# Kernel optimization log

Measured on AMD Instinct MI355X. Metric: run time of the kernel, lower is better.

The kernel has to match this reference:

```python
import jax, jax.numpy as jnp
import numpy as np

H = 512      # hidden_size
NH = 8       # num_heads
DH = H // NH # head_dim = 64
NL = 2       # num_layers
R = 64       # number of AST relation types
PAD = 0      # padding relation index
FF = 4 * H   # FFN inner dim
B, T, S = 4, 512, 512
NEG = -1e10
EPS = 1e-5


def layer_norm(x, g, b):
    m = jnp.mean(x, axis=-1, keepdims=True)
    v = jnp.mean((x - m) ** 2, axis=-1, keepdims=True)
    return (x - m) * jax.lax.rsqrt(v + EPS) * g + b


def setup_inputs() -> dict:
    key = jax.random.key(0)
    ks = iter(jax.random.split(key, 40))

    def n(shape, scale=0.02):
        return jax.random.normal(next(ks), shape, dtype=jnp.float32) * scale

    inp = {
        'q': jax.random.normal(next(ks), (B, T, H), dtype=jnp.float32),
        'kv': jax.random.normal(next(ks), (B, S, H), dtype=jnp.float32),
        'rel_emb_k': n((R, DH)).at[PAD].set(0.0),
        'rel_emb_v': n((R, DH)).at[PAD].set(0.0),
        'Wq_s': n((NL, H, H)), 'bq_s': jnp.zeros((NL, H)),
        'Wk_s': n((NL, H, H)), 'Wv_s': n((NL, H, H)),
        'Wo_s': n((NL, H, H)), 'bo_s': jnp.zeros((NL, H)),
        'ln1_g': jnp.ones((NL, H)), 'ln1_b': jnp.zeros((NL, H)),
        'Wq_c': n((NL, H, H)), 'bq_c': jnp.zeros((NL, H)),
        'Wk_c': n((NL, H, H)), 'Wv_c': n((NL, H, H)),
        'Wo_c': n((NL, H, H)), 'bo_c': jnp.zeros((NL, H)),
        'ln2_g': jnp.ones((NL, H)), 'ln2_b': jnp.zeros((NL, H)),
        'W1': n((NL, H, FF)), 'b1': jnp.zeros((NL, FF)),
        'W2': n((NL, FF, H)), 'b2': jnp.zeros((NL, H)),
        'ln3_g': jnp.ones((NL, H)), 'ln3_b': jnp.zeros((NL, H)),
        'rel_ids': jax.random.randint(next(ks), (B, T, T), 0, R),
        'enc_mask': jnp.ones((B, S), dtype=bool),
    }
    return inp


def reference(q, kv, rel_emb_k, rel_emb_v,
              Wq_s, bq_s, Wk_s, Wv_s, Wo_s, bo_s, ln1_g, ln1_b,
              Wq_c, bq_c, Wk_c, Wv_c, Wo_c, bo_c, ln2_g, ln2_b,
              W1, b1, W2, b2, ln3_g, ln3_b,
              rel_ids, enc_mask):
    scale = np.sqrt(DH).astype(np.float32)
    # relation embeddings shared across layers/heads: [B,T,T,DH]
    rel_k = rel_emb_k[rel_ids]
    rel_v = rel_emb_v[rel_ids]
    tril = jnp.tril(jnp.ones((T, T), dtype=bool))
    rel_mask = (rel_ids != PAD) & tril[None]

    o = q
    for i in range(NL):
        # --- relation-aware masked self-attention ---
        Q = (o @ Wq_s[i] + bq_s[i]).reshape(B, T, NH, DH)
        K = (o @ Wk_s[i]).reshape(B, T, NH, DH)
        V = (o @ Wv_s[i]).reshape(B, T, NH, DH)
        # Q . (K + rel_k)^T decomposed to avoid materializing [B,NH,T,T,DH]
        e = (jnp.einsum('blhd,bmhd->bhlm', Q, K)
             + jnp.einsum('blhd,blmd->bhlm', Q, rel_k)) / scale
        e = jnp.where(rel_mask[:, None], e, NEG)
        a = jax.nn.softmax(e, axis=-1)
        att = (jnp.einsum('bhlm,bmhd->blhd', a, V)
               + jnp.einsum('bhlm,blmd->blhd', a, rel_v)).reshape(B, T, H)
        o = layer_norm(o + att @ Wo_s[i] + bo_s[i], ln1_g[i], ln1_b[i])

        # --- cross-attention ---
        Qc = (o @ Wq_c[i] + bq_c[i]).reshape(B, T, NH, DH)
        Kc = (kv @ Wk_c[i]).reshape(B, S, NH, DH)
        Vc = (kv @ Wv_c[i]).reshape(B, S, NH, DH)
        ec = jnp.einsum('bthd,bshd->bhts', Qc, Kc) / scale
        ec = jnp.where(enc_mask[:, None, None, :], ec, NEG)
        ac = jax.nn.softmax(ec, axis=-1)
        oc = jnp.einsum('bhts,bshd->bthd', ac, Vc).reshape(B, T, H)
        o = layer_norm(o + oc @ Wo_c[i] + bo_c[i], ln2_g[i], ln2_b[i])

        # --- feedforward ---
        h = jax.nn.relu(o @ W1[i] + b1[i])
        o = layer_norm(o + h @ W2[i] + b2[i], ln3_g[i], ln3_b[i])
    return o
```

## Files before the change

kernel.cpp:

```cpp
#include <hip/hip_runtime.h>

static constexpr int Hc  = 512;
static constexpr int NHc = 8;
static constexpr int DHc = 64;
static constexpr int NLc = 2;
static constexpr int Rc  = 64;
static constexpr int FFc = 2048;
static constexpr int Bc  = 4;
static constexpr int Tc  = 512;
#define NEGV (-1e10f)
#define EPSV 1e-5f
#define THRV 6.0f

typedef unsigned short u16;
typedef __attribute__((ext_vector_type(8))) short s16x8;
typedef __attribute__((ext_vector_type(4))) float f32x4;

__device__ __forceinline__ f32x4 mfma_bf16(s16x8 a, s16x8 b, f32x4 c) {
  return __builtin_amdgcn_mfma_f32_16x16x32_bf16(a, b, c, 0, 0, 0);
}
__device__ __forceinline__ u16 f2bf(float f) {
  union { float f; unsigned u; } x; x.f = f;
  unsigned r = (x.u + 0x7FFFu + ((x.u >> 16) & 1u)) >> 16;
  return (u16)r;
}
__device__ __forceinline__ float bf2f(u16 h) {
  union { unsigned u; float f; } x; x.u = ((unsigned)h) << 16;
  return x.f;
}
__device__ __forceinline__ unsigned cvtpk(float a, float b) {
  unsigned r;
  asm("v_cvt_pk_bf16_f32 %0, %1, %2" : "=v"(r) : "v"(a), "v"(b));
  return r;
}

template <int BM, int BN, bool RELU, int OUT>
__global__ __launch_bounds__(256) void gemm_mfma(
    const u16* __restrict__ A, const u16* __restrict__ Wt,
    const float* __restrict__ bias, int biasN,
    void* __restrict__ Cout, int N, int K) {
  __shared__ u16 As[BM * 32];
  __shared__ u16 Bs[BN * 32];
  const int tid = threadIdx.x;
  const int w = tid >> 6, lane = tid & 63, g = lane >> 4, li = lane & 15;
  const int bn = blockIdx.x * BN, bm = blockIdx.y * BM;
  const int r0 = (w & 1) * (BM / 2), c0 = (w >> 1) * (BN / 2);
  constexpr int MR = BM / 32, NR = BN / 32;
  f32x4 acc[MR][NR];
#pragma unroll
  for (int i = 0; i < MR; ++i)
#pragma unroll
    for (int j = 0; j < NR; ++j) acc[i][j] = (f32x4){0.f, 0.f, 0.f, 0.f};

  for (int k0 = 0; k0 < K; k0 += 32) {
    __syncthreads();
#pragma unroll
    for (int it = 0; it < BM / 64; ++it) {
      int s = it * 256 + tid;
      int row = s >> 2, ch = s & 3;
      s16x8 v = *(const s16x8*)(A + (size_t)(bm + row) * K + k0 + ch * 8);
      *(s16x8*)&As[row * 32 + ((ch ^ (row & 3)) * 8)] = v;
    }
#pragma unroll
    for (int it = 0; it < BN / 64; ++it) {
      int s = it * 256 + tid;
      int row = s >> 2, ch = s & 3;
      s16x8 v = *(const s16x8*)(Wt + (size_t)(bn + row) * K + k0 + ch * 8);
      *(s16x8*)&Bs[row * 32 + ((ch ^ (row & 3)) * 8)] = v;
    }
    __syncthreads();
    s16x8 ar[MR], br[NR];
#pragma unroll
    for (int i = 0; i < MR; ++i) {
      int row = r0 + i * 16 + li;
      ar[i] = *(const s16x8*)&As[row * 32 + ((g ^ (row & 3)) * 8)];
    }
#pragma unroll
    for (int j = 0; j < NR; ++j) {
      int row = c0 + j * 16 + li;
      br[j] = *(const s16x8*)&Bs[row * 32 + ((g ^ (row & 3)) * 8)];
    }
#pragma unroll
    for (int i = 0; i < MR; ++i)
#pragma unroll
      for (int j = 0; j < NR; ++j) acc[i][j] = mfma_bf16(ar[i], br[j], acc[i][j]);
  }

#pragma unroll
  for (int j = 0; j < NR; ++j) {
    int col = bn + c0 + j * 16 + li;
    float bv = (bias && col < biasN) ? bias[col] : 0.f;
#pragma unroll
    for (int i = 0; i < MR; ++i) {
#pragma unroll
      for (int r = 0; r < 4; ++r) {
        int rowg = bm + r0 + i * 16 + 4 * g + r;
        float v = acc[i][j][r] + bv;
        if (RELU) v = fmaxf(v, 0.f);
        if (OUT == 0) ((float*)Cout)[(size_t)rowg * N + col] = v;
        else          ((u16*)Cout)[(size_t)rowg * N + col] = f2bf(v);
      }
    }
  }
}

struct WPtrs { const float* p[10]; };

__global__ __launch_bounds__(256) void wcvt(WPtrs wp, u16* __restrict__ dst) {
  constexpr int NE = 20;
  constexpr int srcIdx[NE] = {0,1,0,1,3,3,4,4,5,5,6,6,7,7,2,2,8,8,9,9};
  constexpr int srcOff[NE] = {0,0,262144,262144,0,262144,0,262144,0,262144,
                              0,262144,0,262144,0,262144,0,1048576,0,1048576};
  constexpr int dstOff[NE] = {0,262144,524288,786432,1048576,1310720,
                              1572864,1835008,2097152,2359296,2621440,2883584,
                              3145728,3407872,3670016,3932160,
                              4194304,5242880,6291456,7340032};
  constexpr int KsA[NE] = {512,512,512,512,512,512,512,512,512,512,
                           512,512,512,512,512,512,512,512,2048,2048};
  constexpr int NsA[NE] = {512,512,512,512,512,512,512,512,512,512,
                           512,512,512,512,512,512,2048,2048,512,512};
  constexpr int tileStart[NE] = {0,64,128,192,256,320,384,448,512,576,
                                 640,704,768,832,896,960,1024,1280,1536,1792};
  __shared__ float ts[64 * 65];
  const int tid = threadIdx.x;
  const int bid = blockIdx.x;
  int e = 0;
#pragma unroll
  for (int i = 1; i < NE; ++i) if (bid >= tileStart[i]) e = i;
  const int t = bid - tileStart[e];
  const int Ks_ = KsA[e], Ns_ = NsA[e];
  const int tn = t % (Ns_ >> 6), tk = t / (Ns_ >> 6);
  const float* src = wp.p[srcIdx[e]] + srcOff[e];

  {
    int r = tid >> 2, cb = (tid & 3) * 16;
    const float* sp = src + (size_t)(tk * 64 + r) * Ns_ + tn * 64 + cb;
#pragma unroll
    for (int j = 0; j < 4; ++j) {
      float4 v = ((const float4*)sp)[j];
      float* d = &ts[r * 65 + cb + j * 4];
      d[0] = v.x; d[1] = v.y; d[2] = v.z; d[3] = v.w;
    }
  }
  __syncthreads();
  {
    int n = tid >> 2, kb = (tid & 3) * 16;
    u16* dp = dst + dstOff[e] + (size_t)(tn * 64 + n) * Ks_ + tk * 64 + kb;
    s16x8 o0, o1;
#pragma unroll
    for (int j = 0; j < 8; ++j) o0[j] = (short)f2bf(ts[(kb + j) * 65 + n]);
#pragma unroll
    for (int j = 0; j < 8; ++j) o1[j] = (short)f2bf(ts[(kb + 8 + j) * 65 + n]);
    *(s16x8*)dp = o0;
    *(s16x8*)(dp + 8) = o1;
  }
}

__global__ __launch_bounds__(256) void acvt(
    const float* __restrict__ q, const float* __restrict__ kv,
    const float* __restrict__ relv,
    u16* __restrict__ obf, u16* __restrict__ kvbf, u16* __restrict__ relvt) {
  int bid = blockIdx.x, tid = threadIdx.x;
  if (bid == 1024) {
    int d = tid >> 2, rb = (tid & 3) * 16;
    s16x8 o0, o1;
#pragma unroll
    for (int j = 0; j < 8; ++j) o0[j] = (short)f2bf(relv[(rb + j) * 64 + d]);
#pragma unroll
    for (int j = 0; j < 8; ++j) o1[j] = (short)f2bf(relv[(rb + 8 + j) * 64 + d]);
    *(s16x8*)(relvt + d * 64 + rb) = o0;
    *(s16x8*)(relvt + d * 64 + rb + 8) = o1;
    return;
  }
  int i = bid * 256 + tid;
  const float* src; u16* dst; size_t off;
  if (i < 131072) { src = q; dst = obf; off = (size_t)i * 8; }
  else { src = kv; dst = kvbf; off = (size_t)(i - 131072) * 8; }
  float4 a = *(const float4*)(src + off);
  float4 b = *(const float4*)(src + off + 4);
  s16x8 o;
  o[0] = (short)f2bf(a.x); o[1] = (short)f2bf(a.y);
  o[2] = (short)f2bf(a.z); o[3] = (short)f2bf(a.w);
  o[4] = (short)f2bf(b.x); o[5] = (short)f2bf(b.y);
  o[6] = (short)f2bf(b.z); o[7] = (short)f2bf(b.w);
  *(s16x8*)(dst + off) = o;
}

__global__ __launch_bounds__(256) void qr_kernel(
    const u16* __restrict__ Q, const float* __restrict__ relk,
    float* __restrict__ Qr) {
  __shared__ float rk[64 * 65];
  __shared__ float qs[4][64];
  const int tid = threadIdx.x;
  {
    int r = tid >> 2, cb = (tid & 3) * 16;
    const float* sp = relk + r * 64 + cb;
#pragma unroll
    for (int j = 0; j < 4; ++j) {
      float4 v = ((const float4*)sp)[j];
      float* d = &rk[r * 65 + cb + j * 4];
      d[0] = v.x; d[1] = v.y; d[2] = v.z; d[3] = v.w;
    }
  }
  const int sub = tid >> 6, r = tid & 63;
  const int unit = blockIdx.x * 4 + sub;
  qs[sub][r] = bf2f(Q[(size_t)(unit >> 3) * 1024 + (unit & 7) * 64 + r]);
  __syncthreads();
  float acc = 0.f;
#pragma unroll
  for (int d = 0; d < 64; ++d) acc += qs[sub][d] * rk[r * 65 + d];
  Qr[(size_t)unit * 64 + r] = acc;
}

#define RELID(RV, r) ((r) == 0 ? (RV).x : (r) == 1 ? (RV).y : (r) == 2 ? (RV).z : (RV).w)

#define LOADKREL(KF, RF, C8) do {                                              \
    _Pragma("unroll") for (int mt = 0; mt < 4; ++mt) {                         \
      KF[mt * 2 + 0] = *(const s16x8*)(kp + (size_t)(C8) * 65536 + mt * 16384);\
      KF[mt * 2 + 1] = *(const s16x8*)(kp + (size_t)(C8) * 65536 + mt * 16384 + 32); \
      RF[mt] = *(const int4*)(rp + (C8) * 64 + mt * 16);                       \
    } } while (0)

#define COMPUTE_SELF(KF, RF, C8) do {                                          \
    s16x8 vf[8];                                                               \
    _Pragma("unroll") for (int df = 0; df < 4; ++df) {                         \
      vf[df * 2 + 0] = *(const s16x8*)(vp + (size_t)(C8) * 64 + df * 32768);   \
      vf[df * 2 + 1] = *(const s16x8*)(vp + (size_t)(C8) * 64 + df * 32768 + 32); } \
    f32x4 sf[4];                                                               \
    _Pragma("unroll") for (int mt = 0; mt < 4; ++mt) {                         \
      sf[mt] = (f32x4){0.f, 0.f, 0.f, 0.f};                                    \
      sf[mt] = mfma_bf16(KF[mt * 2 + 0], aq0, sf[mt]);                         \
      sf[mt] = mfma_bf16(KF[mt * 2 + 1], aq1, sf[mt]); }                       \
    float p[4][4];                                                             \
    float pmax = NEGV;                                                         \
    _Pragma("unroll") for (int mt = 0; mt < 4; ++mt) {                         \
      _Pragma("unroll") for (int r = 0; r < 4; ++r) {                          \
        int rel = RELID(RF[mt], r);                                            \
        bool valid = (rel != 0) && ((C8) * 64 + mt * 16 + 4 * g + r <= lrow);  \
        p[mt][r] = valid ? (sf[mt][r] + qrs[li * 66 + rel]) * 0.125f : NEGV;   \
        pmax = fmaxf(pmax, p[mt][r]); } }                                      \
    pmax = fmaxf(pmax, __shfl_xor(pmax, 16));                                  \
    pmax = fmaxf(pmax, __shfl_xor(pmax, 32));                                  \
    if (__any(pmax > mrow + THRV)) {                                           \
      float mnew = (pmax > mrow + THRV) ? pmax : mrow;                         \
      float f = __expf(mrow - mnew);                                           \
      rsum *= f;                                                               \
      _Pragma("unroll") for (int j = 0; j < 8; ++j) {                          \
        float2* p2 = (float2*)&bk[li * 66 + g * 16 + 2 * j];                   \
        float2 v = *p2; v.x *= f; v.y *= f; *p2 = v; }                         \
      _Pragma("unroll") for (int r = 0; r < 4; ++r) {                          \
        float fr = __shfl(f, 4 * g + r);                                       \
        _Pragma("unroll") for (int df = 0; df < 4; ++df) oacc[df][r] *= fr; }  \
      mrow = mnew; }                                                           \
    unsigned pk[4][2];                                                         \
    _Pragma("unroll") for (int mt = 0; mt < 4; ++mt) {                         \
      _Pragma("unroll") for (int r = 0; r < 4; ++r) {                          \
        float pv = __expf(p[mt][r] - mrow);                                    \
        p[mt][r] = pv;                                                         \
        rsum += pv;                                                            \
        if (pv > 0.f) atomicAdd(&bk[li * 66 + RELID(RF[mt], r)], pv); }        \
      pk[mt][0] = cvtpk(p[mt][0], p[mt][1]);                                   \
      pk[mt][1] = cvtpk(p[mt][2], p[mt][3]); }                                 \
    _Pragma("unroll") for (int kk = 0; kk < 2; ++kk) {                         \
      union { s16x8 v; unsigned u[4]; } pa;                                    \
      _Pragma("unroll") for (int q = 0; q < 4; ++q) {                          \
        int src = ((2 * (g & 1) + (q >> 1)) << 4) + li;                        \
        unsigned uA = __shfl(pk[2 * kk][q & 1], src);                          \
        unsigned uB = __shfl(pk[2 * kk + 1][q & 1], src);                      \
        pa.u[q] = (g < 2) ? uA : uB; }                                         \
      _Pragma("unroll") for (int df = 0; df < 4; ++df)                         \
        oacc[df] = mfma_bf16(pa.v, vf[df * 2 + kk], oacc[df]); }               \
  } while (0)

__global__ __launch_bounds__(64) void attn_self_part(
    const u16* __restrict__ Qb, const u16* __restrict__ Kb,
    const u16* __restrict__ VT,
    const float* __restrict__ Qr, const int* __restrict__ rel_ids,
    const u16* __restrict__ relvt,
    float* __restrict__ po, float2* __restrict__ pms) {
  __shared__ float qrs[16 * 66];
  __shared__ float buck[16 * 66];
  float* bk = buck;

  const int lane = threadIdx.x;
  const int g = lane >> 4, li = lane & 15;
  const int qt = blockIdx.x, h = blockIdx.y;
  const int b = blockIdx.z >> 2, s = blockIdx.z & 3;
  const int lrow = qt * 16 + li;
  const int growq = b * 512 + qt * 16;

  const u16* qp = Qb + (size_t)(growq + li) * 1024 + h * 64;
  s16x8 aq0 = *(const s16x8*)(qp + g * 8);
  s16x8 aq1 = *(const s16x8*)(qp + 32 + g * 8);
  const u16* kp = Kb + (size_t)(b * 512 + li) * 1024 + h * 64 + g * 8;
  const u16* vp = VT + (size_t)(h * 64 + li) * 2048 + b * 512 + g * 8;
  const int* rp = rel_ids + (size_t)(growq + li) * 512 + 4 * g;

#pragma unroll
  for (int j = 0; j < 4; ++j) {
    int fi = j * 64 + lane;
    int row = fi >> 4, c4 = (fi & 15) * 4;
    float4 v = *(const float4*)(Qr + ((size_t)(growq + row) * 8 + h) * 64 + c4);
    *(float4*)&qrs[row * 66 + c4] = v;
    *(float4*)&buck[row * 66 + c4] = make_float4(0.f, 0.f, 0.f, 0.f);
  }

  float mrow = NEGV, rsum = 0.f;
  f32x4 oacc[4];
#pragma unroll
  for (int d = 0; d < 4; ++d) oacc[d] = (f32x4){0.f, 0.f, 0.f, 0.f};

  {
    s16x8 kA[8]; int4 rA[4];
    LOADKREL(kA, rA, 2 * s);
    COMPUTE_SELF(kA, rA, 2 * s);
  }
  {
    s16x8 kA[8]; int4 rA[4];
    LOADKREL(kA, rA, 2 * s + 1);
    COMPUTE_SELF(kA, rA, 2 * s + 1);
  }

  rsum += __shfl_xor(rsum, 16);
  rsum += __shfl_xor(rsum, 32);

#pragma unroll
  for (int kk = 0; kk < 2; ++kk) {
    float bb[8];
#pragma unroll
    for (int j = 0; j < 4; ++j) {
      float2 v = *(const float2*)&bk[li * 66 + kk * 32 + g * 8 + 2 * j];
      bb[2 * j] = v.x; bb[2 * j + 1] = v.y;
    }
    union { s16x8 v; unsigned u[4]; } pb;
#pragma unroll
    for (int q = 0; q < 4; ++q) pb.u[q] = cvtpk(bb[2 * q], bb[2 * q + 1]);
#pragma unroll
    for (int df = 0; df < 4; ++df) {
      s16x8 rb = *(const s16x8*)(relvt + (df * 16 + li) * 64 + kk * 32 + g * 8);
      oacc[df] = mfma_bf16(pb.v, rb, oacc[df]);
    }
  }

  const size_t idx = (size_t)(b * 8 + h) * 512 + qt * 16;
#pragma unroll
  for (int df = 0; df < 4; ++df)
#pragma unroll
    for (int r = 0; r < 4; ++r)
      po[((idx + 4 * g + r) * 4 + s) * 64 + df * 16 + li] = oacc[df][r];
  if (lane < 16) pms[(idx + lane) * 4 + s] = make_float2(mrow, rsum);
}

#define LOADK_X(KF, C8) do {                                                   \
    _Pragma("unroll") for (int mt = 0; mt < 4; ++mt) {                         \
      KF[mt * 2 + 0] = *(const s16x8*)(kp + (size_t)(C8) * 65536 + mt * 16384);\
      KF[mt * 2 + 1] = *(const s16x8*)(kp + (size_t)(C8) * 65536 + mt * 16384 + 32); \
    } } while (0)

#define COMPUTE_X(KF, C8) do {                                                 \
    s16x8 vf[8];                                                               \
    _Pragma("unroll") for (int df = 0; df < 4; ++df) {                         \
      vf[df * 2 + 0] = *(const s16x8*)(vp + (size_t)(C8) * 64 + df * 32768);   \
      vf[df * 2 + 1] = *(const s16x8*)(vp + (size_t)(C8) * 64 + df * 32768 + 32); } \
    f32x4 sf[4];                                                               \
    _Pragma("unroll") for (int mt = 0; mt < 4; ++mt) {                         \
      sf[mt] = (f32x4){0.f, 0.f, 0.f, 0.f};                                    \
      sf[mt] = mfma_bf16(KF[mt * 2 + 0], aq0, sf[mt]);                         \
      sf[mt] = mfma_bf16(KF[mt * 2 + 1], aq1, sf[mt]); }                       \
    float p[4][4];                                                             \
    float pmax = NEGV;                                                         \
    _Pragma("unroll") for (int mt = 0; mt < 4; ++mt)                           \
      _Pragma("unroll") for (int r = 0; r < 4; ++r) {                          \
        p[mt][r] = sf[mt][r] * 0.125f;                                         \
        pmax = fmaxf(pmax, p[mt][r]); }                                        \
    pmax = fmaxf(pmax, __shfl_xor(pmax, 16));                                  \
    pmax = fmaxf(pmax, __shfl_xor(pmax, 32));                                  \
    if (__any(pmax > mrow + THRV)) {                                           \
      float mnew = (pmax > mrow + THRV) ? pmax : mrow;                         \
      float f = __expf(mrow - mnew);                                           \
      rsum *= f;                                                               \
      _Pragma("unroll") for (int r = 0; r < 4; ++r) {                          \
        float fr = __shfl(f, 4 * g + r);                                       \
        _Pragma("unroll") for (int df = 0; df < 4; ++df) oacc[df][r] *= fr; }  \
      mrow = mnew; }                                                           \
    unsigned pk[4][2];                                                         \
    _Pragma("unroll") for (int mt = 0; mt < 4; ++mt) {                         \
      _Pragma("unroll") for (int r = 0; r < 4; ++r) {                          \
        float pv = __expf(p[mt][r] - mrow);                                    \
        p[mt][r] = pv;                                                         \
        rsum += pv; }                                                          \
      pk[mt][0] = cvtpk(p[mt][0], p[mt][1]);                                   \
      pk[mt][1] = cvtpk(p[mt][2], p[mt][3]); }                                 \
    _Pragma("unroll") for (int kk = 0; kk < 2; ++kk) {                         \
      union { s16x8 v; unsigned u[4]; } pa;                                    \
      _Pragma("unroll") for (int q = 0; q < 4; ++q) {                          \
        int src = ((2 * (g & 1) + (q >> 1)) << 4) + li;                        \
        unsigned uA = __shfl(pk[2 * kk][q & 1], src);                          \
        unsigned uB = __shfl(pk[2 * kk + 1][q & 1], src);                      \
        pa.u[q] = (g < 2) ? uA : uB; }                                         \
      _Pragma("unroll") for (int df = 0; df < 4; ++df)                         \
        oacc[df] = mfma_bf16(pa.v, vf[df * 2 + kk], oacc[df]); }               \
  } while (0)

__global__ __launch_bounds__(64) void attn_cross_part(
    const u16* __restrict__ Qb,
    const u16* __restrict__ Kb,
    const u16* __restrict__ VT,
    float* __restrict__ po, float2* __restrict__ pms) {
  const int lane = threadIdx.x;
  const int g = lane >> 4, li = lane & 15;
  const int qt = blockIdx.x, h = blockIdx.y;
  const int b = blockIdx.z >> 2, s = blockIdx.z & 3;
  const int growq = b * 512 + qt * 16;

  const u16* qp = Qb + (size_t)(growq + li) * 512 + h * 64;
  s16x8 aq0 = *(const s16x8*)(qp + g * 8);
  s16x8 aq1 = *(const s16x8*)(qp + 32 + g * 8);
  const u16* kp = Kb + (size_t)(b * 512 + li) * 1024 + h * 64 + g * 8;
  const u16* vp = VT + (size_t)(h * 64 + li) * 2048 + b * 512 + g * 8;

  float mrow = NEGV, rsum = 0.f;
  f32x4 oacc[4];
#pragma unroll
  for (int d = 0; d < 4; ++d) oacc[d] = (f32x4){0.f, 0.f, 0.f, 0.f};

  {
    s16x8 kA[8];
    LOADK_X(kA, 2 * s);
    COMPUTE_X(kA, 2 * s);
  }
  {
    s16x8 kA[8];
    LOADK_X(kA, 2 * s + 1);
    COMPUTE_X(kA, 2 * s + 1);
  }

  rsum += __shfl_xor(rsum, 16);
  rsum += __shfl_xor(rsum, 32);

  const size_t idx = (size_t)(b * 8 + h) * 512 + qt * 16;
#pragma unroll
  for (int df = 0; df < 4; ++df)
#pragma unroll
    for (int r = 0; r < 4; ++r)
      po[((idx + 4 * g + r) * 4 + s) * 64 + df * 16 + li] = oacc[df][r];
  if (lane < 16) pms[(idx + lane) * 4 + s] = make_float2(mrow, rsum);
}

__global__ __launch_bounds__(256) void attn_merge(
    const float* __restrict__ po, const float2* __restrict__ pms,
    u16* __restrict__ att) {
  const int t = threadIdx.x;
  const size_t idx = (size_t)blockIdx.x * 16 + (t >> 4);
  const int d4 = (t & 15) * 4;
  float2 ms[4];
  float m = NEGV;
#pragma unroll
  for (int s = 0; s < 4; ++s) {
    ms[s] = pms[idx * 4 + s];
    m = fmaxf(m, ms[s].x);
  }
  float rs = 0.f;
  float4 o = make_float4(0.f, 0.f, 0.f, 0.f);
#pragma unroll
  for (int s = 0; s < 4; ++s) {
    float f = __expf(ms[s].x - m);
    rs += f * ms[s].y;
    float4 v = *(const float4*)(po + (idx * 4 + s) * 64 + d4);
    o.x += f * v.x; o.y += f * v.y; o.z += f * v.z; o.w += f * v.w;
  }
  const float inv = 1.f / rs;
  const int b = (int)(idx >> 12), h = (int)(idx >> 9) & 7, row = (int)(idx & 511);
  ushort4 ov;
  ov.x = f2bf(o.x * inv);
  ov.y = f2bf(o.y * inv);
  ov.z = f2bf(o.z * inv);
  ov.w = f2bf(o.w * inv);
  *(ushort4*)(att + (size_t)(b * 512 + row) * 512 + h * 64 + d4) = ov;
}

__global__ __launch_bounds__(256) void ln_res(
    const float* __restrict__ x, const float* __restrict__ dlt,
    const float* __restrict__ g, const float* __restrict__ bta,
    float* __restrict__ out, u16* __restrict__ obf) {
  __shared__ float red_s[256];
  const int row = blockIdx.x, tid = threadIdx.x;
  const size_t base = (size_t)row * Hc;
  float v0 = x[base + tid] + dlt[base + tid];
  float v1 = x[base + tid + 256] + dlt[base + tid + 256];

  red_s[tid] = v0 + v1;
  __syncthreads();
  for (int s = 128; s > 0; s >>= 1) {
    if (tid < s) red_s[tid] += red_s[tid + s];
    __syncthreads();
  }
  const float mean = red_s[0] * (1.f / Hc);
  __syncthreads();
  const float d0 = v0 - mean, d1 = v1 - mean;
  red_s[tid] = d0 * d0 + d1 * d1;
  __syncthreads();
  for (int s = 128; s > 0; s >>= 1) {
    if (tid < s) red_s[tid] += red_s[tid + s];
    __syncthreads();
  }
  const float rstd = rsqrtf(red_s[0] * (1.f / Hc) + EPSV);
  float o0 = d0 * rstd * g[tid] + bta[tid];
  float o1 = d1 * rstd * g[tid + 256] + bta[tid + 256];
  out[base + tid] = o0;
  out[base + tid + 256] = o1;
  obf[base + tid] = f2bf(o0);
  obf[base + tid + 256] = f2bf(o1);
}

extern "C" void kernel_launch(void* const* d_in, const int* in_sizes, int n_in,
                              void* d_out, int out_size, void* d_ws, size_t ws_size,
                              hipStream_t stream) {
  const float* q    = (const float*)d_in[0];
  const float* kv   = (const float*)d_in[1];
  const float* relk = (const float*)d_in[2];
  const float* relv = (const float*)d_in[3];
  const float* Wq_s = (const float*)d_in[4];
  const float* bq_s = (const float*)d_in[5];
  const float* Wk_s = (const float*)d_in[6];
  const float* Wv_s = (const float*)d_in[7];
  const float* Wo_s = (const float*)d_in[8];
  const float* bo_s = (const float*)d_in[9];
  const float* ln1g = (const float*)d_in[10];
  const float* ln1b = (const float*)d_in[11];
  const float* Wq_c = (const float*)d_in[12];
  const float* bq_c = (const float*)d_in[13];
  const float* Wk_c = (const float*)d_in[14];
  const float* Wv_c = (const float*)d_in[15];
  const float* Wo_c = (const float*)d_in[16];
  const float* bo_c = (const float*)d_in[17];
  const float* ln2g = (const float*)d_in[18];
  const float* ln2b = (const float*)d_in[19];
  const float* W1   = (const float*)d_in[20];
  const float* b1   = (const float*)d_in[21];
  const float* W2   = (const float*)d_in[22];
  const float* b2   = (const float*)d_in[23];
  const float* ln3g = (const float*)d_in[24];
  const float* ln3b = (const float*)d_in[25];
  const int*   rel  = (const int*)d_in[26];

  char* wsb = (char*)d_ws;
  const size_t NT = (size_t)Bc * Tc;
  float* o     = (float*)wsb;  wsb += NT * Hc * 4;
  float* bDlt  = (float*)wsb;  wsb += NT * Hc * 4;
  float* Qr    = (float*)wsb;  wsb += NT * 8 * 64 * 4;
  u16* obf     = (u16*)wsb;    wsb += NT * Hc * 2;
  u16* kvbf    = (u16*)wsb;    wsb += NT * Hc * 2;
  u16* bQK     = (u16*)wsb;    wsb += NT * 1024 * 2;
  u16* bVt     = (u16*)wsb;    wsb += (size_t)512 * 2048 * 2;
  u16* bQc     = (u16*)wsb;    wsb += NT * Hc * 2;
  u16* bKc     = (u16*)wsb;    wsb += NT * 1024 * 2;
  u16* bVtc    = (u16*)wsb;    wsb += (size_t)1024 * 2048 * 2;
  u16* bAtt    = (u16*)wsb;    wsb += NT * Hc * 2;
  u16* bH      = (u16*)wsb;    wsb += NT * FFc * 2;
  u16* relvt   = (u16*)wsb;    wsb += 64 * 64 * 2;
  u16* wbuf    = (u16*)wsb;    wsb += (size_t)8388608 * 2;
  float* po    = (float*)wsb;  wsb += (size_t)16384 * 4 * 64 * 4;
  float2* pms  = (float2*)wsb; wsb += (size_t)16384 * 4 * 8;

  WPtrs wp;
  wp.p[0] = Wq_s; wp.p[1] = Wk_s; wp.p[2] = Wv_s; wp.p[3] = Wo_s;
  wp.p[4] = Wq_c; wp.p[5] = Wk_c; wp.p[6] = Wv_c; wp.p[7] = Wo_c;
  wp.p[8] = W1;   wp.p[9] = W2;

  dim3 blk(256);
  wcvt<<<dim3(2048), blk, 0, stream>>>(wp, wbuf);
  acvt<<<dim3(1025), blk, 0, stream>>>(q, kv, relv, obf, kvbf, relvt);
  hipMemcpyAsync(o, q, NT * Hc * 4, hipMemcpyDeviceToDevice, stream);

  gemm_mfma<64, 128, false, 1><<<dim3(8, 32), blk, 0, stream>>>(
      kvbf, wbuf + 2097152, nullptr, 0, bKc, 1024, 512);
  gemm_mfma<64, 128, false, 1><<<dim3(16, 16), blk, 0, stream>>>(
      wbuf + 2621440, kvbf, nullptr, 0, bVtc, 2048, 512);

  const dim3 gLN(NT);
  const dim3 gPART(32, 8, 16);
  const dim3 gMERGE(1024);
  for (int i = 0; i < NLc; ++i) {
    gemm_mfma<64, 128, false, 1><<<dim3(8, 32), blk, 0, stream>>>(
        obf, wbuf + (size_t)i * 524288, bq_s + i * Hc, Hc, bQK, 1024, 512);
    gemm_mfma<64, 64, false, 1><<<dim3(32, 8), blk, 0, stream>>>(
        wbuf + 3670016 + (size_t)i * 262144, obf, nullptr, 0, bVt, 2048, 512);
    qr_kernel<<<dim3(4096), blk, 0, stream>>>(bQK, relk, Qr);
    attn_self_part<<<gPART, dim3(64), 0, stream>>>(
        bQK, bQK + 512, bVt, Qr, rel, relvt, po, pms);
    attn_merge<<<gMERGE, blk, 0, stream>>>(po, pms, bAtt);
    gemm_mfma<64, 64, false, 0><<<dim3(8, 32), blk, 0, stream>>>(
        bAtt, wbuf + 1048576 + (size_t)i * 262144, bo_s + i * Hc, Hc, bDlt, Hc, 512);
    ln_res<<<gLN, blk, 0, stream>>>(o, bDlt, ln1g + i * Hc, ln1b + i * Hc, o, obf);

    gemm_mfma<64, 64, false, 1><<<dim3(8, 32), blk, 0, stream>>>(
        obf, wbuf + 1572864 + (size_t)i * 262144, bq_c + i * Hc, Hc, bQc, Hc, 512);
    attn_cross_part<<<gPART, dim3(64), 0, stream>>>(
        bQc, bKc + i * 512, bVtc + (size_t)i * 512 * 2048, po, pms);
    attn_merge<<<gMERGE, blk, 0, stream>>>(po, pms, bAtt);
    gemm_mfma<64, 64, false, 0><<<dim3(8, 32), blk, 0, stream>>>(
        bAtt, wbuf + 3145728 + (size_t)i * 262144, bo_c + i * Hc, Hc, bDlt, Hc, 512);
    ln_res<<<gLN, blk, 0, stream>>>(o, bDlt, ln2g + i * Hc, ln2b + i * Hc, o, obf);

    gemm_mfma<128, 128, true, 1><<<dim3(16, 16), blk, 0, stream>>>(
        obf, wbuf + 4194304 + (size_t)i * 1048576, b1 + i * FFc, FFc, bH, FFc, 512);
    gemm_mfma<64, 64, false, 0><<<dim3(8, 32), blk, 0, stream>>>(
        bH, wbuf + 6291456 + (size_t)i * 1048576, b2 + i * Hc, Hc, bDlt, Hc, 2048);
    float* lnout = (i == NLc - 1) ? (float*)d_out : o;
    ln_res<<<gLN, blk, 0, stream>>>(o, bDlt, ln3g + i * Hc, ln3b + i * Hc, lnout, obf);
  }
}
```

Measured before the change: 441.3 us.

## Prefetch GEMM tiles in registers, compress rel ids to u8 and Qr to bf16

The GEMM kernel now prefetches the next K-slice into registers while the current tile is in shared memory, which overlaps global loads with MFMA work. Relation ids are packed once into a u8 buffer, and the Q·relk table is stored as bf16, which shrinks the bytes the self-attention kernel reads. Both attention kernels issue the loads for their two key chunks before computing either, and the FFN-up GEMM switches to a 64x128 tile for more blocks. The costs are extra registers, one extra conversion pass over rel_ids, and bf16 rounding of the relation logits.

```diff
diff --git a/kernel.cpp b/kernel.cpp
--- a/kernel.cpp
+++ b/kernel.cpp
@@ -13,6 +13,7 @@
 #define THRV 6.0f
 
 typedef unsigned short u16;
+typedef unsigned char u8;
 typedef __attribute__((ext_vector_type(8))) short s16x8;
 typedef __attribute__((ext_vector_type(4))) float f32x4;
 
@@ -46,27 +47,48 @@
   const int bn = blockIdx.x * BN, bm = blockIdx.y * BM;
   const int r0 = (w & 1) * (BM / 2), c0 = (w >> 1) * (BN / 2);
   constexpr int MR = BM / 32, NR = BN / 32;
+  constexpr int AIT = BM / 64, BIT = BN / 64;
   f32x4 acc[MR][NR];
 #pragma unroll
   for (int i = 0; i < MR; ++i)
 #pragma unroll
     for (int j = 0; j < NR; ++j) acc[i][j] = (f32x4){0.f, 0.f, 0.f, 0.f};
+
+  s16x8 va[AIT], vb[BIT];
+#pragma unroll
+  for (int it = 0; it < AIT; ++it) {
+    int s = it * 256 + tid, row = s >> 2, ch = s & 3;
+    va[it] = *(const s16x8*)(A + (size_t)(bm + row) * K + ch * 8);
+  }
+#pragma unroll
+  for (int it = 0; it < BIT; ++it) {
+    int s = it * 256 + tid, row = s >> 2, ch = s & 3;
+    vb[it] = *(const s16x8*)(Wt + (size_t)(bn + row) * K + ch * 8);
+  }
 
   for (int k0 = 0; k0 < K; k0 += 32) {
     __syncthreads();
 #pragma unroll
-    for (int it = 0; it < BM / 64; ++it) {
-      int s = it * 256 + tid;
-      int row = s >> 2, ch = s & 3;
-      s16x8 v = *(const s16x8*)(A + (size_t)(bm + row) * K + k0 + ch * 8);
-      *(s16x8*)&As[row * 32 + ((ch ^ (row & 3)) * 8)] = v;
-    }
-#pragma unroll
-    for (int it = 0; it < BN / 64; ++it) {
-      int s = it * 256 + tid;
-      int row = s >> 2, ch = s & 3;
-      s16x8 v = *(const s16x8*)(Wt + (size_t)(bn + row) * K + k0 + ch * 8);
-      *(s16x8*)&Bs[row * 32 + ((ch ^ (row & 3)) * 8)] = v;
+    for (int it = 0; it < AIT; ++it) {
+      int s = it * 256 + tid, row = s >> 2, ch = s & 3;
+      *(s16x8*)&As[row * 32 + ((ch ^ (row & 3)) * 8)] = va[it];
+    }
+#pragma unroll
+    for (int it = 0; it < BIT; ++it) {
+      int s = it * 256 + tid, row = s >> 2, ch = s & 3;
+      *(s16x8*)&Bs[row * 32 + ((ch ^ (row & 3)) * 8)] = vb[it];
+    }
+    if (k0 + 32 < K) {
+#pragma unroll
+      for (int it = 0; it < AIT; ++it) {
+        int s = it * 256 + tid, row = s >> 2, ch = s & 3;
+        va[it] = *(const s16x8*)(A + (size_t)(bm + row) * K + k0 + 32 + ch * 8);
+      }
+#pragma unroll
+      for (int it = 0; it < BIT; ++it) {
+        int s = it * 256 + tid, row = s >> 2, ch = s & 3;
+        vb[it] = *(const s16x8*)(Wt + (size_t)(bn + row) * K + k0 + 32 + ch * 8);
+      }
     }
     __syncthreads();
     s16x8 ar[MR], br[NR];
@@ -158,9 +180,21 @@
 
 __global__ __launch_bounds__(256) void acvt(
     const float* __restrict__ q, const float* __restrict__ kv,
-    const float* __restrict__ relv,
-    u16* __restrict__ obf, u16* __restrict__ kvbf, u16* __restrict__ relvt) {
+    const float* __restrict__ relv, const int* __restrict__ rel,
+    u16* __restrict__ obf, u16* __restrict__ kvbf, u16* __restrict__ relvt,
+    u8* __restrict__ rel8) {
   int bid = blockIdx.x, tid = threadIdx.x;
+  if (bid >= 1025) {
+    size_t i = (size_t)(bid - 1025) * 2048 + (size_t)tid * 8;
+    int4 a = *(const int4*)(rel + i);
+    int4 b = *(const int4*)(rel + i + 4);
+    unsigned lo = (unsigned)(a.x & 255) | ((unsigned)(a.y & 255) << 8) |
+                  ((unsigned)(a.z & 255) << 16) | ((unsigned)(a.w & 255) << 24);
+    unsigned hi = (unsigned)(b.x & 255) | ((unsigned)(b.y & 255) << 8) |
+                  ((unsigned)(b.z & 255) << 16) | ((unsigned)(b.w & 255) << 24);
+    *(uint2*)(rel8 + i) = make_uint2(lo, hi);
+    return;
+  }
   if (bid == 1024) {
     int d = tid >> 2, rb = (tid & 3) * 16;
     s16x8 o0, o1;
@@ -188,7 +222,7 @@
 
 __global__ __launch_bounds__(256) void qr_kernel(
     const u16* __restrict__ Q, const float* __restrict__ relk,
-    float* __restrict__ Qr) {
+    u16* __restrict__ Qr) {
   __shared__ float rk[64 * 65];
   __shared__ float qs[4][64];
   const int tid = threadIdx.x;
@@ -209,16 +243,14 @@
   float acc = 0.f;
 #pragma unroll
   for (int d = 0; d < 64; ++d) acc += qs[sub][d] * rk[r * 65 + d];
-  Qr[(size_t)unit * 64 + r] = acc;
-}
-
-#define RELID(RV, r) ((r) == 0 ? (RV).x : (r) == 1 ? (RV).y : (r) == 2 ? (RV).z : (RV).w)
+  Qr[(size_t)unit * 64 + r] = f2bf(acc);
+}
 
 #define LOADKREL(KF, RF, C8) do {                                              \
     _Pragma("unroll") for (int mt = 0; mt < 4; ++mt) {                         \
       KF[mt * 2 + 0] = *(const s16x8*)(kp + (size_t)(C8) * 65536 + mt * 16384);\
       KF[mt * 2 + 1] = *(const s16x8*)(kp + (size_t)(C8) * 65536 + mt * 16384 + 32); \
-      RF[mt] = *(const int4*)(rp + (C8) * 64 + mt * 16);                       \
+      RF[mt] = *(const unsigned*)(rp8 + (C8) * 64 + mt * 16);                  \
     } } while (0)
 
 #define COMPUTE_SELF(KF, RF, C8) do {                                          \
@@ -232,10 +264,12 @@
       sf[mt] = mfma_bf16(KF[mt * 2 + 0], aq0, sf[mt]);                         \
       sf[mt] = mfma_bf16(KF[mt * 2 + 1], aq1, sf[mt]); }                       \
     float p[4][4];                                                             \
+    int rl[4][4];                                                              \
     float pmax = NEGV;                                                         \
     _Pragma("unroll") for (int mt = 0; mt < 4; ++mt) {                         \
       _Pragma("unroll") for (int r = 0; r < 4; ++r) {                          \
-        int rel = RELID(RF[mt], r);                                            \
+        int rel = (int)((RF[mt] >> (8 * r)) & 255u);                           \
+        rl[mt][r] = rel;                                                       \
         bool valid = (rel != 0) && ((C8) * 64 + mt * 16 + 4 * g + r <= lrow);  \
         p[mt][r] = valid ? (sf[mt][r] + qrs[li * 66 + rel]) * 0.125f : NEGV;   \
         pmax = fmaxf(pmax, p[mt][r]); } }                                      \
@@ -258,7 +292,7 @@
         float pv = __expf(p[mt][r] - mrow);                                    \
         p[mt][r] = pv;                                                         \
         rsum += pv;                                                            \
-        if (pv > 0.f) atomicAdd(&bk[li * 66 + RELID(RF[mt], r)], pv); }        \
+        if (pv > 0.f) atomicAdd(&bk[li * 66 + rl[mt][r]], pv); }               \
       pk[mt][0] = cvtpk(p[mt][0], p[mt][1]);                                   \
       pk[mt][1] = cvtpk(p[mt][2], p[mt][3]); }                                 \
     _Pragma("unroll") for (int kk = 0; kk < 2; ++kk) {                         \
@@ -275,7 +309,7 @@
 __global__ __launch_bounds__(64) void attn_self_part(
     const u16* __restrict__ Qb, const u16* __restrict__ Kb,
     const u16* __restrict__ VT,
-    const float* __restrict__ Qr, const int* __restrict__ rel_ids,
+    const u16* __restrict__ Qrb, const u8* __restrict__ rel8,
     const u16* __restrict__ relvt,
     float* __restrict__ po, float2* __restrict__ pms) {
   __shared__ float qrs[16 * 66];
@@ -294,15 +328,23 @@
   s16x8 aq1 = *(const s16x8*)(qp + 32 + g * 8);
   const u16* kp = Kb + (size_t)(b * 512 + li) * 1024 + h * 64 + g * 8;
   const u16* vp = VT + (size_t)(h * 64 + li) * 2048 + b * 512 + g * 8;
-  const int* rp = rel_ids + (size_t)(growq + li) * 512 + 4 * g;
-
-#pragma unroll
-  for (int j = 0; j < 4; ++j) {
-    int fi = j * 64 + lane;
-    int row = fi >> 4, c4 = (fi & 15) * 4;
-    float4 v = *(const float4*)(Qr + ((size_t)(growq + row) * 8 + h) * 64 + c4);
-    *(float4*)&qrs[row * 66 + c4] = v;
-    *(float4*)&buck[row * 66 + c4] = make_float4(0.f, 0.f, 0.f, 0.f);
+  const u8* rp8 = rel8 + (size_t)(growq + li) * 512 + 4 * g;
+
+  {
+    int row = lane >> 2, c16 = (lane & 3) * 16;
+    const u16* qrp = Qrb + ((size_t)(growq + row) * 8 + h) * 64 + c16;
+    s16x8 v0 = *(const s16x8*)qrp;
+    s16x8 v1 = *(const s16x8*)(qrp + 8);
+#pragma unroll
+    for (int j = 0; j < 8; ++j) {
+      qrs[row * 66 + c16 + j] = bf2f((u16)v0[j]);
+      qrs[row * 66 + c16 + 8 + j] = bf2f((u16)v1[j]);
+    }
+#pragma unroll
+    for (int j = 0; j < 5; ++j) {
+      int fid = j * 64 + lane;
+      if (fid < 264) *(float4*)&buck[fid * 4] = make_float4(0.f, 0.f, 0.f, 0.f);
+    }
   }
 
   float mrow = NEGV, rsum = 0.f;
@@ -310,16 +352,12 @@
 #pragma unroll
   for (int d = 0; d < 4; ++d) oacc[d] = (f32x4){0.f, 0.f, 0.f, 0.f};
 
-  {
-    s16x8 kA[8]; int4 rA[4];
-    LOADKREL(kA, rA, 2 * s);
-    COMPUTE_SELF(kA, rA, 2 * s);
-  }
-  {
-    s16x8 kA[8]; int4 rA[4];
-    LOADKREL(kA, rA, 2 * s + 1);
-    COMPUTE_SELF(kA, rA, 2 * s + 1);
-  }
+  s16x8 kA[8], kB[8];
+  unsigned rA[4], rB[4];
+  LOADKREL(kA, rA, 2 * s);
+  LOADKREL(kB, rB, 2 * s + 1);
+  COMPUTE_SELF(kA, rA, 2 * s);
+  COMPUTE_SELF(kB, rB, 2 * s + 1);
 
   rsum += __shfl_xor(rsum, 16);
   rsum += __shfl_xor(rsum, 32);
@@ -424,16 +462,11 @@
 #pragma unroll
   for (int d = 0; d < 4; ++d) oacc[d] = (f32x4){0.f, 0.f, 0.f, 0.f};
 
-  {
-    s16x8 kA[8];
-    LOADK_X(kA, 2 * s);
-    COMPUTE_X(kA, 2 * s);
-  }
-  {
-    s16x8 kA[8];
-    LOADK_X(kA, 2 * s + 1);
-    COMPUTE_X(kA, 2 * s + 1);
-  }
+  s16x8 kA[8], kB[8];
+  LOADK_X(kA, 2 * s);
+  LOADK_X(kB, 2 * s + 1);
+  COMPUTE_X(kA, 2 * s);
+  COMPUTE_X(kB, 2 * s + 1);
 
   rsum += __shfl_xor(rsum, 16);
   rsum += __shfl_xor(rsum, 32);
@@ -548,7 +581,7 @@
   const size_t NT = (size_t)Bc * Tc;
   float* o     = (float*)wsb;  wsb += NT * Hc * 4;
   float* bDlt  = (float*)wsb;  wsb += NT * Hc * 4;
-  float* Qr    = (float*)wsb;  wsb += NT * 8 * 64 * 4;
+  u16* Qr      = (u16*)wsb;    wsb += NT * 8 * 64 * 2;
   u16* obf     = (u16*)wsb;    wsb += NT * Hc * 2;
   u16* kvbf    = (u16*)wsb;    wsb += NT * Hc * 2;
   u16* bQK     = (u16*)wsb;    wsb += NT * 1024 * 2;
@@ -559,6 +592,7 @@
   u16* bAtt    = (u16*)wsb;    wsb += NT * Hc * 2;
   u16* bH      = (u16*)wsb;    wsb += NT * FFc * 2;
   u16* relvt   = (u16*)wsb;    wsb += 64 * 64 * 2;
+  u8* rel8     = (u8*)wsb;     wsb += (size_t)NT * 512;
   u16* wbuf    = (u16*)wsb;    wsb += (size_t)8388608 * 2;
   float* po    = (float*)wsb;  wsb += (size_t)16384 * 4 * 64 * 4;
   float2* pms  = (float2*)wsb; wsb += (size_t)16384 * 4 * 8;
@@ -570,7 +604,7 @@
 
   dim3 blk(256);
   wcvt<<<dim3(2048), blk, 0, stream>>>(wp, wbuf);
-  acvt<<<dim3(1025), blk, 0, stream>>>(q, kv, relv, obf, kvbf, relvt);
+  acvt<<<dim3(1537), blk, 0, stream>>>(q, kv, relv, rel, obf, kvbf, relvt, rel8);
   hipMemcpyAsync(o, q, NT * Hc * 4, hipMemcpyDeviceToDevice, stream);
 
   gemm_mfma<64, 128, false, 1><<<dim3(8, 32), blk, 0, stream>>>(
@@ -588,7 +622,7 @@
         wbuf + 3670016 + (size_t)i * 262144, obf, nullptr, 0, bVt, 2048, 512);
     qr_kernel<<<dim3(4096), blk, 0, stream>>>(bQK, relk, Qr);
     attn_self_part<<<gPART, dim3(64), 0, stream>>>(
-        bQK, bQK + 512, bVt, Qr, rel, relvt, po, pms);
+        bQK, bQK + 512, bVt, Qr, rel8, relvt, po, pms);
     attn_merge<<<gMERGE, blk, 0, stream>>>(po, pms, bAtt);
     gemm_mfma<64, 64, false, 0><<<dim3(8, 32), blk, 0, stream>>>(
         bAtt, wbuf + 1048576 + (size_t)i * 262144, bo_s + i * Hc, Hc, bDlt, Hc, 512);
@@ -603,7 +637,7 @@
         bAtt, wbuf + 3145728 + (size_t)i * 262144, bo_c + i * Hc, Hc, bDlt, Hc, 512);
     ln_res<<<gLN, blk, 0, stream>>>(o, bDlt, ln2g + i * Hc, ln2b + i * Hc, o, obf);
 
-    gemm_mfma<128, 128, true, 1><<<dim3(16, 16), blk, 0, stream>>>(
+    gemm_mfma<64, 128, true, 1><<<dim3(16, 32), blk, 0, stream>>>(
         obf, wbuf + 4194304 + (size_t)i * 1048576, b1 + i * FFc, FFc, bH, FFc, 512);
     gemm_mfma<64, 64, false, 0><<<dim3(8, 32), blk, 0, stream>>>(
         bH, wbuf + 6291456 + (size_t)i * 1048576, b2 + i * Hc, Hc, bDlt, Hc, 2048);
```

Measured after the change: 389.4 us. 1.13x faster.
